# Performance work log

Measured on AMD Instinct MI355X. Metric: run time of the kernel, lower is better.

The kernel has to match this reference:

```python
import jax, jax.numpy as jnp
import numpy as np

B, S, D = 4, 2048, 512
E, K = 8, 2
MH = 4 * D      # resmlp mlp hidden
EH = 2 * D      # expert hidden
EPS = 1e-5


def setup_inputs() -> dict:
    key = jax.random.key(0)
    ks = jax.random.split(key, 16)
    s = 0.02
    return {
        "x": jax.random.normal(ks[0], (B, S, D), dtype=jnp.float32),
        "ln1_g": jnp.ones((D,), jnp.float32), "ln1_b": jnp.zeros((D,), jnp.float32),
        "w1": jax.random.normal(ks[1], (D, MH), jnp.float32) * s,
        "b1": jnp.zeros((MH,), jnp.float32),
        "w2": jax.random.normal(ks[2], (MH, D), jnp.float32) * s,
        "b2": jnp.zeros((D,), jnp.float32),
        "ln2_g": jnp.ones((D,), jnp.float32), "ln2_b": jnp.zeros((D,), jnp.float32),
        "wr": jax.random.normal(ks[3], (E, D), jnp.float32) * s,
        "ew1": jax.random.normal(ks[4], (E, D, EH), jnp.float32) * s,
        "eb1": jnp.zeros((E, EH), jnp.float32),
        "ew2": jax.random.normal(ks[5], (E, EH, D), jnp.float32) * s,
        "eb2": jnp.zeros((E, D), jnp.float32),
        "lnf_g": jnp.ones((D,), jnp.float32), "lnf_b": jnp.zeros((D,), jnp.float32),
    }


def _ln(z, g, b):
    m = z.mean(-1, keepdims=True)
    v = ((z - m) ** 2).mean(-1, keepdims=True)
    return (z - m) * jax.lax.rsqrt(v + EPS) * g + b


def reference(x, ln1_g, ln1_b, w1, b1, w2, b2, ln2_g, ln2_b,
              wr, ew1, eb1, ew2, eb2, lnf_g, lnf_b):
    # ---- ResidualMLPBlock (eval mode: dropout is identity) ----
    h = _ln(x, ln1_g, ln1_b)
    h = jax.nn.gelu(h @ w1 + b1, approximate=False) @ w2 + b2
    x = x + h
    x = _ln(x, ln2_g, ln2_b) + x
    # ---- MoE (eval: no jitter noise, aux_loss = 0) ----
    xf = x.reshape(-1, D)              # [N, D], N = B*S
    n = xf.shape[0]
    probs = jax.nn.softmax(xf @ wr.T, axis=-1)          # [N, E]
    topv, topi = jax.lax.top_k(probs, K)                # [N, K]
    topv = topv / topv.sum(-1, keepdims=True)
    # dense per-token gate per expert: sum over k of renormalized prob where idx==j
    gates = jnp.zeros((n, E), xf.dtype).at[jnp.arange(n)[:, None], topi].add(topv)
    # per-expert MLP over all tokens (masked scatter-combine via gates)
    he = jax.nn.gelu(jnp.einsum("nd,edh->enh", xf, ew1) + eb1[:, None, :],
                     approximate=False)                 # [E, N, 2D]
    ye = jnp.einsum("enh,ehd->end", he, ew2) + eb2[:, None, :]  # [E, N, D]
    out = jnp.einsum("ne,end->nd", gates, ye).reshape(B, S, D)
    # ---- final LayerNorm ----
    out = _ln(out, lnf_g, lnf_b)
    aux_loss = jnp.zeros((), x.dtype)  # eval mode
    return out, aux_loss
```

## Files before the change

kernel.cpp:

```cpp
#include <hip/hip_runtime.h>

#define NTOK 8192
#define DIM  512
#define MHID 2048
#define EHID 1024
#define NEXP 8
#define RBLK 64

using half_t = _Float16;
typedef _Float16 f16x8 __attribute__((ext_vector_type(8)));
typedef float    f32x16 __attribute__((ext_vector_type(16)));

#define MFMA32(a, b, c) __builtin_amdgcn_mfma_f32_32x32x16_f16((a), (b), (c), 0, 0, 0)

typedef const __attribute__((address_space(1))) void* gas_ptr;
typedef __attribute__((address_space(3))) void*       las_ptr;
__device__ __forceinline__ void gl16(const void* g, void* l) {
    __builtin_amdgcn_global_load_lds((gas_ptr)g, (las_ptr)l, 16, 0, 0);
}

__device__ __forceinline__ float gelu_exact(float v) {
    return 0.5f * v * (1.0f + erff(v * 0.70710678118654752f));
}

__device__ __forceinline__ float block_sum4(float v, float* red, int tid) {
#pragma unroll
    for (int off = 32; off; off >>= 1) v += __shfl_down(v, off);
    if ((tid & 63) == 0) red[tid >> 6] = v;
    __syncthreads();
    float r = red[0] + red[1] + red[2] + red[3];
    __syncthreads();
    return r;
}

__global__ __launch_bounds__(256) void ln1_split_kernel(
    const float* __restrict__ x, const float* __restrict__ g, const float* __restrict__ b,
    half_t* __restrict__ xh, half_t* __restrict__ xl)
{
    const int row = blockIdx.x, tid = threadIdx.x;
    __shared__ float red[4];
    const size_t base = (size_t)row * DIM;
    float2 v = reinterpret_cast<const float2*>(x + base)[tid];
    float mean = block_sum4(v.x + v.y, red, tid) * (1.0f / DIM);
    float d0 = v.x - mean, d1 = v.y - mean;
    float var = block_sum4(d0 * d0 + d1 * d1, red, tid) * (1.0f / DIM);
    float rstd = rsqrtf(var + 1e-5f);
    int d = tid * 2;
    float y0 = d0 * rstd * g[d]     + b[d];
    float y1 = d1 * rstd * g[d + 1] + b[d + 1];
    half_t h0 = (half_t)y0, h1 = (half_t)y1;
    xh[base + d] = h0;  xh[base + d + 1] = h1;
    xl[base + d]     = (half_t)(y0 - (float)h0);
    xl[base + d + 1] = (half_t)(y1 - (float)h1);
}

__global__ __launch_bounds__(256) void resid_ln2_kernel(
    const float* __restrict__ x, float* __restrict__ p0, const float* __restrict__ p1,
    const float* __restrict__ b2,
    const float* __restrict__ g, const float* __restrict__ b,
    half_t* __restrict__ x3h)
{
    const int row = blockIdx.x, tid = threadIdx.x;
    __shared__ float red[4];
    const size_t base = (size_t)row * DIM;
    float2 xv = reinterpret_cast<const float2*>(x + base)[tid];
    float2 h0 = reinterpret_cast<float2*>(p0 + base)[tid];
    float2 h1 = reinterpret_cast<const float2*>(p1 + base)[tid];
    float2 bb = reinterpret_cast<const float2*>(b2)[tid];
    float z0 = xv.x + h0.x + h1.x + bb.x, z1 = xv.y + h0.y + h1.y + bb.y;
    float mean = block_sum4(z0 + z1, red, tid) * (1.0f / DIM);
    float d0 = z0 - mean, d1 = z1 - mean;
    float var = block_sum4(d0 * d0 + d1 * d1, red, tid) * (1.0f / DIM);
    float rstd = rsqrtf(var + 1e-5f);
    int d = tid * 2;
    float y0 = d0 * rstd * g[d]     + b[d]     + z0;
    float y1 = d1 * rstd * g[d + 1] + b[d + 1] + z1;
    float2 o; o.x = y0; o.y = y1;
    reinterpret_cast<float2*>(p0 + base)[tid] = o;
    x3h[base + d]     = (half_t)y0;
    x3h[base + d + 1] = (half_t)y1;
}

__global__ void transpose_split_kernel(const float* __restrict__ in,
                                       half_t* __restrict__ oh, half_t* __restrict__ ol,
                                       int R, int C)
{
    __shared__ float t[32][33];
    const size_t mo = (size_t)blockIdx.z * (size_t)R * (size_t)C;
    const int c0 = blockIdx.x * 32, r0 = blockIdx.y * 32;
    const int tx = threadIdx.x, ty = threadIdx.y;
    for (int i = ty; i < 32; i += 8) t[i][tx] = in[mo + (size_t)(r0 + i) * C + c0 + tx];
    __syncthreads();
    for (int i = ty; i < 32; i += 8) {
        float v = t[tx][i];
        size_t o = mo + (size_t)(c0 + i) * R + r0 + tx;
        half_t h = (half_t)v;
        oh[o] = h;
        if (ol) ol[o] = (half_t)(v - (float)h);
    }
}

template <int EPI, int NREP>
__global__ __launch_bounds__(512, 2) void gemm8_kernel(
    const half_t* __restrict__ A0, const half_t* __restrict__ A1,
    const half_t* __restrict__ B0, const half_t* __restrict__ B1,
    const float* __restrict__ bias,
    float* __restrict__ Cf0, float* __restrict__ Cf1,
    half_t* __restrict__ Ch, half_t* __restrict__ Cl,
    int Nc, int K, int Ktile)
{
    constexpr int BN    = NREP * 128;
    constexpr int LOADS = 4 + 2 * NREP;
    constexpr int TOT   = 16384 + NREP * 8192;
    __shared__ __align__(16) half_t lds[2 * TOT];

    const int m0 = blockIdx.x * 256, n0 = blockIdx.y * BN;
    const int kbeg = blockIdx.z * Ktile;
    float* Cf = blockIdx.z ? Cf1 : Cf0;
    const int tid = threadIdx.x;
    const int lane = tid & 63, wid = tid >> 6;
    const int wr = wid >> 2, wc = wid & 3;
    const int l31 = lane & 31, l5 = lane >> 5;

    const half_t* gsrc[LOADS];
    {
        const half_t* A0p = A0 + (size_t)m0 * K + kbeg;
        const half_t* A1p = A1 + (size_t)m0 * K + kbeg;
        const half_t* B0p = B0 + (size_t)n0 * K + kbeg;
        const half_t* B1p = B1 + (size_t)n0 * K + kbeg;
#pragma unroll
        for (int i = 0; i < LOADS; i++) {
            int c = tid + 512 * i;
            const half_t* base; int cm;
            if (c < 1024)                  { base = A0p; cm = c; }
            else if (c < 2048)             { base = A1p; cm = c - 1024; }
            else if (c < 2048 + NREP * 512){ base = B0p; cm = c - 2048; }
            else                           { base = B1p; cm = c - 2048 - NREP * 512; }
            int r = cm >> 2, ss = (cm & 3) ^ ((r >> 1) & 3);
            gsrc[i] = base + (size_t)r * K + ss * 8;
        }
    }

    int oa[4][2], ob[NREP][2];
#pragma unroll
    for (int m = 0; m < 4; m++)
#pragma unroll
        for (int kh = 0; kh < 2; kh++) {
            int ra = wr * 128 + m * 32 + l31;
            oa[m][kh] = ra * 32 + (((l5 + 2 * kh) ^ ((ra >> 1) & 3)) << 3);
        }
#pragma unroll
    for (int n = 0; n < NREP; n++)
#pragma unroll
        for (int kh = 0; kh < 2; kh++) {
            int rb = wc * (NREP * 32) + n * 32 + l31;
            ob[n][kh] = rb * 32 + (((l5 + 2 * kh) ^ ((rb >> 1) & 3)) << 3);
        }

    f32x16 acc[4][NREP];
#pragma unroll
    for (int m = 0; m < 4; m++)
#pragma unroll
        for (int n = 0; n < NREP; n++)
#pragma unroll
            for (int q = 0; q < 16; q++) acc[m][n][q] = 0.f;

    auto stage = [&](int bsel, int kof) {
#pragma unroll
        for (int i = 0; i < LOADS; i++)
            gl16(gsrc[i] + kof, &lds[bsel * TOT + (tid + 512 * i) * 8]);
    };
    auto phase = [&](int p, int kh) {
        const half_t* buf = &lds[p ? TOT : 0];
        f16x8 ah[4], al[4], bh[NREP], bl[NREP];
#pragma unroll
        for (int m = 0; m < 4; m++) {
            ah[m] = *(const f16x8*)(buf + oa[m][kh]);
            al[m] = *(const f16x8*)(buf + 8192 + oa[m][kh]);
        }
#pragma unroll
        for (int n = 0; n < NREP; n++) {
            bh[n] = *(const f16x8*)(buf + 16384 + ob[n][kh]);
            bl[n] = *(const f16x8*)(buf + 16384 + BN * 32 + ob[n][kh]);
        }
        __builtin_amdgcn_s_setprio(1);
#pragma unroll
        for (int m = 0; m < 4; m++)
#pragma unroll
            for (int n = 0; n < NREP; n++) {
                acc[m][n] = MFMA32(ah[m], bh[n], acc[m][n]);
                acc[m][n] = MFMA32(al[m], bh[n], acc[m][n]);
                acc[m][n] = MFMA32(ah[m], bl[n], acc[m][n]);
            }
        __builtin_amdgcn_s_setprio(0);
    };

    const int nsteps = Ktile / 32;
    stage(0, 0);
#pragma unroll 1
    for (int s = 0; s < nsteps - 1; ++s) {
        stage((s + 1) & 1, (s + 1) * 32);
        if constexpr (NREP == 2) asm volatile("s_waitcnt vmcnt(8)" ::: "memory");
        else                     asm volatile("s_waitcnt vmcnt(6)" ::: "memory");
        __builtin_amdgcn_s_barrier();
        phase(s & 1, 0);
        __builtin_amdgcn_s_barrier();
        phase(s & 1, 1);
        __builtin_amdgcn_s_barrier();
    }
    asm volatile("s_waitcnt vmcnt(0)" ::: "memory");
    __builtin_amdgcn_s_barrier();
    phase((nsteps - 1) & 1, 0);
    __builtin_amdgcn_s_barrier();
    phase((nsteps - 1) & 1, 1);

    const int er = 4 * l5;
#pragma unroll
    for (int m = 0; m < 4; m++)
#pragma unroll
        for (int n = 0; n < NREP; n++) {
            int cc = n0 + wc * (NREP * 32) + n * 32 + l31;
            float bv = (EPI == 1) ? bias[cc] : 0.f;
#pragma unroll
            for (int reg = 0; reg < 16; reg++) {
                int rr = m0 + wr * 128 + m * 32 + er + 8 * (reg >> 2) + (reg & 3);
                float v = acc[m][n][reg] + bv;
                size_t o = (size_t)rr * Nc + cc;
                if (EPI == 1) {
                    float ge = gelu_exact(v);
                    half_t h = (half_t)ge;
                    Ch[o] = h;
                    Cl[o] = (half_t)(ge - (float)h);
                } else {
                    Cf[o] = v;
                }
            }
        }
}

__global__ __launch_bounds__(256) void router_kernel(
    const float* __restrict__ x3, const float* __restrict__ wrm,
    int* __restrict__ cnt, int* __restrict__ aid, float* __restrict__ gate)
{
    __shared__ float wl[NEXP][DIM];
    __shared__ int   texp[RBLK * 2];
    __shared__ float tgate[RBLK * 2];
    __shared__ int   lslot[RBLK * 2];
    __shared__ int   lcnt[NEXP], lbase[NEXP];
    const int tid = threadIdx.x;
    for (int i = tid; i < NEXP * DIM / 4; i += 256)
        reinterpret_cast<float4*>(&wl[0][0])[i] = reinterpret_cast<const float4*>(wrm)[i];
    if (tid < NEXP) lcnt[tid] = 0;
    __syncthreads();
    const int w = tid >> 6, lane = tid & 63;
#pragma unroll 1
    for (int t = 0; t < RBLK / 4; ++t) {
        const int lt = w * (RBLK / 4) + t;
        const int token = blockIdx.x * RBLK + lt;
        const float* xr = x3 + (size_t)token * DIM;
        float a[NEXP];
#pragma unroll
        for (int e = 0; e < NEXP; e++) a[e] = 0.f;
#pragma unroll
        for (int d0 = 0; d0 < DIM; d0 += 64) {
            float xv = xr[d0 + lane];
#pragma unroll
            for (int e = 0; e < NEXP; e++) a[e] += xv * wl[e][d0 + lane];
        }
#pragma unroll
        for (int e = 0; e < NEXP; e++)
#pragma unroll
            for (int off = 32; off; off >>= 1) a[e] += __shfl_xor(a[e], off);
        if (lane == 0) {
            int i1 = 0; float v1 = a[0];
#pragma unroll
            for (int e = 1; e < NEXP; e++) if (a[e] > v1) { v1 = a[e]; i1 = e; }
            int i2 = -1; float v2 = -3.4e38f;
#pragma unroll
            for (int e = 0; e < NEXP; e++) if (e != i1 && a[e] > v2) { v2 = a[e]; i2 = e; }
            float e2 = expf(v2 - v1);
            float g1 = 1.0f / (1.0f + e2);
            texp[lt * 2]      = i1; tgate[lt * 2]      = g1;
            texp[lt * 2 + 1]  = i2; tgate[lt * 2 + 1]  = 1.0f - g1;
        }
    }
    __syncthreads();
    if (tid < RBLK * 2) lslot[tid] = atomicAdd(&lcnt[texp[tid]], 1);
    __syncthreads();
    if (tid < NEXP) lbase[tid] = atomicAdd(&cnt[tid * 32], lcnt[tid]);
    __syncthreads();
    if (tid < RBLK * 2) {
        const int e = texp[tid];
        const int asg = blockIdx.x * (RBLK * 2) + tid;
        aid[e * NTOK + lbase[e] + lslot[tid]] = asg;
        gate[asg] = tgate[tid];
    }
}

__global__ __launch_bounds__(256) void egemm1_kernel(
    const half_t* __restrict__ X,
    const half_t* __restrict__ W,
    const float* __restrict__ eb1,
    const int* __restrict__ cnt, const int* __restrict__ aid,
    half_t* __restrict__ He)
{
    const int bid = blockIdx.x;
    const int e = bid >> 9, rem = bid & 511;
    const int mt = rem >> 3, nt = rem & 7;
    const int ne = cnt[e * 32];
    if (mt * 128 >= ne) return;
    __shared__ __align__(16) half_t As[2][128 * 32];
    __shared__ __align__(16) half_t Bs[2][128 * 32];
    __shared__ int rowmap[128];
    const int tid = threadIdx.x;
    if (tid < 128) {
        int slot = mt * 128 + tid;
        rowmap[tid] = (slot < ne) ? aid[e * NTOK + slot] : -1;
    }
    __syncthreads();
    const int lane = tid & 63, wid = tid >> 6;
    const int wr = wid >> 1, wc = wid & 1;
    const int c0 = tid, c1 = tid + 256;
    const int r0 = c0 >> 2, s0 = (c0 & 3) ^ ((r0 >> 1) & 3);
    const int r1 = c1 >> 2, s1 = (c1 & 3) ^ ((r1 >> 1) & 3);
    const int a0r = rowmap[r0], a1r = rowmap[r1];
    const half_t* pa0 = X + (size_t)(a0r >= 0 ? (a0r >> 1) : 0) * DIM + s0 * 8;
    const half_t* pa1 = X + (size_t)(a1r >= 0 ? (a1r >> 1) : 0) * DIM + s1 * 8;
    const half_t* pb0 = W + (size_t)e * EHID * DIM + (size_t)(nt * 128 + r0) * DIM + s0 * 8;
    const half_t* pb1 = W + (size_t)e * EHID * DIM + (size_t)(nt * 128 + r1) * DIM + s1 * 8;

    const int l31 = lane & 31, l5 = lane >> 5;
    int oa[2][2], ob[2][2];
#pragma unroll
    for (int i = 0; i < 2; i++)
#pragma unroll
        for (int kh = 0; kh < 2; kh++) {
            int ra = wr * 64 + i * 32 + l31;
            oa[i][kh] = ra * 32 + (((l5 + kh * 2) ^ ((ra >> 1) & 3)) << 3);
            int rb = wc * 64 + i * 32 + l31;
            ob[i][kh] = rb * 32 + (((l5 + kh * 2) ^ ((rb >> 1) & 3)) << 3);
        }
    f32x16 acc[2][2];
#pragma unroll
    for (int i = 0; i < 2; i++)
#pragma unroll
        for (int j = 0; j < 2; j++)
#pragma unroll
            for (int q = 0; q < 16; q++) acc[i][j][q] = 0.f;

    auto stage = [&](int bsel, int k0) {
        gl16(pa0 + k0, &As[bsel][c0 * 8]);
        gl16(pa1 + k0, &As[bsel][c1 * 8]);
        gl16(pb0 + k0, &Bs[bsel][c0 * 8]);
        gl16(pb1 + k0, &Bs[bsel][c1 * 8]);
    };
    auto compute = [&](int bsel) {
#pragma unroll
        for (int kh = 0; kh < 2; kh++) {
            f16x8 a0 = *(const f16x8*)(&As[bsel][0] + oa[0][kh]);
            f16x8 a1 = *(const f16x8*)(&As[bsel][0] + oa[1][kh]);
            f16x8 b0 = *(const f16x8*)(&Bs[bsel][0] + ob[0][kh]);
            f16x8 b1 = *(const f16x8*)(&Bs[bsel][0] + ob[1][kh]);
            acc[0][0] = MFMA32(a0, b0, acc[0][0]);
            acc[0][1] = MFMA32(a0, b1, acc[0][1]);
            acc[1][0] = MFMA32(a1, b0, acc[1][0]);
            acc[1][1] = MFMA32(a1, b1, acc[1][1]);
        }
    };

    stage(0, 0);
#pragma unroll 1
    for (int k0 = 0; k0 < DIM; k0 += 64) {
        __syncthreads();
        if (k0 + 32 < DIM) stage(1, k0 + 32);
        compute(0);
        __syncthreads();
        if (k0 + 64 < DIM) stage(0, k0 + 64);
        compute(1);
    }
    const int er = 4 * l5;
#pragma unroll
    for (int i = 0; i < 2; i++)
#pragma unroll
        for (int reg = 0; reg < 16; reg++) {
            int rloc = wr * 64 + i * 32 + er + 8 * (reg >> 2) + (reg & 3);
            int a = rowmap[rloc];
            if (a >= 0) {
#pragma unroll
                for (int j = 0; j < 2; j++) {
                    int cc = nt * 128 + wc * 64 + j * 32 + l31;
                    float v = acc[i][j][reg] + eb1[e * EHID + cc];
                    He[(size_t)a * EHID + cc] = (half_t)gelu_exact(v);
                }
            }
        }
}

__global__ __launch_bounds__(256) void egemm2_kernel(
    const half_t* __restrict__ Hin,
    const half_t* __restrict__ W,
    const float* __restrict__ eb2,
    const int* __restrict__ cnt, const int* __restrict__ aid,
    const float* __restrict__ gate,
    float* __restrict__ Ye)
{
    const int bid = blockIdx.x;
    const int e = bid >> 8, rem = bid & 255;
    const int mt = rem >> 2, nt = rem & 3;
    const int ne = cnt[e * 32];
    if (mt * 128 >= ne) return;
    __shared__ __align__(16) half_t As[2][128 * 32];
    __shared__ __align__(16) half_t Bs[2][128 * 32];
    __shared__ int rowmap[128];
    const int tid = threadIdx.x;
    if (tid < 128) {
        int slot = mt * 128 + tid;
        rowmap[tid] = (slot < ne) ? aid[e * NTOK + slot] : -1;
    }
    __syncthreads();
    const int lane = tid & 63, wid = tid >> 6;
    const int wr = wid >> 1, wc = wid & 1;
    const int c0 = tid, c1 = tid + 256;
    const int r0 = c0 >> 2, s0 = (c0 & 3) ^ ((r0 >> 1) & 3);
    const int r1 = c1 >> 2, s1 = (c1 & 3) ^ ((r1 >> 1) & 3);
    const int a0r = rowmap[r0], a1r = rowmap[r1];
    const half_t* pa0 = Hin + (size_t)(a0r >= 0 ? a0r : 0) * EHID + s0 * 8;
    const half_t* pa1 = Hin + (size_t)(a1r >= 0 ? a1r : 0) * EHID + s1 * 8;
    const half_t* pb0 = W + (size_t)e * DIM * EHID + (size_t)(nt * 128 + r0) * EHID + s0 * 8;
    const half_t* pb1 = W + (size_t)e * DIM * EHID + (size_t)(nt * 128 + r1) * EHID + s1 * 8;

    const int l31 = lane & 31, l5 = lane >> 5;
    int oa[2][2], ob[2][2];
#pragma unroll
    for (int i = 0; i < 2; i++)
#pragma unroll
        for (int kh = 0; kh < 2; kh++) {
            int ra = wr * 64 + i * 32 + l31;
            oa[i][kh] = ra * 32 + (((l5 + kh * 2) ^ ((ra >> 1) & 3)) << 3);
            int rb = wc * 64 + i * 32 + l31;
            ob[i][kh] = rb * 32 + (((l5 + kh * 2) ^ ((rb >> 1) & 3)) << 3);
        }
    f32x16 acc[2][2];
#pragma unroll
    for (int i = 0; i < 2; i++)
#pragma unroll
        for (int j = 0; j < 2; j++)
#pragma unroll
            for (int q = 0; q < 16; q++) acc[i][j][q] = 0.f;

    auto stage = [&](int bsel, int k0) {
        gl16(pa0 + k0, &As[bsel][c0 * 8]);
        gl16(pa1 + k0, &As[bsel][c1 * 8]);
        gl16(pb0 + k0, &Bs[bsel][c0 * 8]);
        gl16(pb1 + k0, &Bs[bsel][c1 * 8]);
    };
    auto compute = [&](int bsel) {
#pragma unroll
        for (int kh = 0; kh < 2; kh++) {
            f16x8 a0 = *(const f16x8*)(&As[bsel][0] + oa[0][kh]);
            f16x8 a1 = *(const f16x8*)(&As[bsel][0] + oa[1][kh]);
            f16x8 b0 = *(const f16x8*)(&Bs[bsel][0] + ob[0][kh]);
            f16x8 b1 = *(const f16x8*)(&Bs[bsel][0] + ob[1][kh]);
            acc[0][0] = MFMA32(a0, b0, acc[0][0]);
            acc[0][1] = MFMA32(a0, b1, acc[0][1]);
            acc[1][0] = MFMA32(a1, b0, acc[1][0]);
            acc[1][1] = MFMA32(a1, b1, acc[1][1]);
        }
    };

    stage(0, 0);
#pragma unroll 1
    for (int k0 = 0; k0 < EHID; k0 += 64) {
        __syncthreads();
        if (k0 + 32 < EHID) stage(1, k0 + 32);
        compute(0);
        __syncthreads();
        if (k0 + 64 < EHID) stage(0, k0 + 64);
        compute(1);
    }
    const int er = 4 * l5;
#pragma unroll
    for (int i = 0; i < 2; i++)
#pragma unroll
        for (int reg = 0; reg < 16; reg++) {
            int rloc = wr * 64 + i * 32 + er + 8 * (reg >> 2) + (reg & 3);
            int a = rowmap[rloc];
            if (a >= 0) {
                float gv = gate[a];
#pragma unroll
                for (int j = 0; j < 2; j++) {
                    int cc = nt * 128 + wc * 64 + j * 32 + l31;
                    float v = (acc[i][j][reg] + eb2[e * DIM + cc]) * gv;
                    Ye[(size_t)a * DIM + cc] = v;
                }
            }
        }
}

__global__ __launch_bounds__(256) void combine_lnf_kernel(
    const float* __restrict__ Ye, const float* __restrict__ g, const float* __restrict__ b,
    float* __restrict__ out)
{
    const int t = blockIdx.x, tid = threadIdx.x;
    __shared__ float red[4];
    float2 y0 = reinterpret_cast<const float2*>(Ye + (size_t)(2 * t) * DIM)[tid];
    float2 y1 = reinterpret_cast<const float2*>(Ye + (size_t)(2 * t + 1) * DIM)[tid];
    float z0 = y0.x + y1.x, z1 = y0.y + y1.y;
    float mean = block_sum4(z0 + z1, red, tid) * (1.0f / DIM);
    float d0 = z0 - mean, d1 = z1 - mean;
    float var = block_sum4(d0 * d0 + d1 * d1, red, tid) * (1.0f / DIM);
    float rstd = rsqrtf(var + 1e-5f);
    int d = tid * 2;
    out[(size_t)t * DIM + d]     = d0 * rstd * g[d]     + b[d];
    out[(size_t)t * DIM + d + 1] = d1 * rstd * g[d + 1] + b[d + 1];
    if (t == 0 && tid == 0) out[(size_t)NTOK * DIM] = 0.f;
}

__global__ void zero_cnt_kernel(int* cnt) {
    cnt[threadIdx.x] = 0;
}

extern "C" void kernel_launch(void* const* d_in, const int* in_sizes, int n_in,
                              void* d_out, int out_size, void* d_ws, size_t ws_size,
                              hipStream_t stream)
{
    (void)in_sizes; (void)n_in; (void)out_size; (void)ws_size;
    const float* x    = (const float*)d_in[0];
    const float* ln1g = (const float*)d_in[1];
    const float* ln1b = (const float*)d_in[2];
    const float* w1   = (const float*)d_in[3];
    const float* b1   = (const float*)d_in[4];
    const float* w2   = (const float*)d_in[5];
    const float* b2   = (const float*)d_in[6];
    const float* ln2g = (const float*)d_in[7];
    const float* ln2b = (const float*)d_in[8];
    const float* wrm  = (const float*)d_in[9];
    const float* ew1  = (const float*)d_in[10];
    const float* eb1  = (const float*)d_in[11];
    const float* ew2  = (const float*)d_in[12];
    const float* eb2  = (const float*)d_in[13];
    const float* lnfg = (const float*)d_in[14];
    const float* lnfb = (const float*)d_in[15];
    float* out = (float*)d_out;

    char* w = (char*)d_ws;
    size_t off = 0;
    auto take = [&](size_t bytes) {
        char* p = w + off;
        off += bytes;
        off = (off + 255) & ~(size_t)255;
        return p;
    };
    half_t* xh_h  = (half_t*)take((size_t)NTOK * DIM * 2);
    half_t* xh_l  = (half_t*)take((size_t)NTOK * DIM * 2);
    half_t* w1t_h = (half_t*)take((size_t)DIM * MHID * 2);
    half_t* w1t_l = (half_t*)take((size_t)DIM * MHID * 2);
    half_t* w2t_h = (half_t*)take((size_t)MHID * DIM * 2);
    half_t* w2t_l = (half_t*)take((size_t)MHID * DIM * 2);
    char*   big   = take((size_t)NTOK * MHID * 2 * 2);
    half_t* a1h   = (half_t*)big;
    half_t* a1l   = (half_t*)(big + (size_t)NTOK * MHID * 2);
    half_t* heh   = (half_t*)big;
    float*  yef   = (float*)(big + (size_t)NTOK * MHID * 2);
    float*  x3f   = (float*)take((size_t)NTOK * DIM * 4);
    half_t* x3h   = (half_t*)take((size_t)NTOK * DIM * 2);
    half_t* ew1t  = (half_t*)take((size_t)NEXP * DIM * EHID * 2);
    half_t* ew2t  = (half_t*)take((size_t)NEXP * EHID * DIM * 2);
    int*    cnt   = (int*)take(1024);
    int*    aid   = (int*)take((size_t)NEXP * NTOK * 4);
    float*  gate  = (float*)take((size_t)NTOK * 2 * 4);

    float* p0 = x3f;
    float* p1 = (float*)xh_h;

    zero_cnt_kernel<<<1, 256, 0, stream>>>(cnt);
    ln1_split_kernel<<<NTOK, 256, 0, stream>>>(x, ln1g, ln1b, xh_h, xh_l);
    transpose_split_kernel<<<dim3(MHID / 32, DIM / 32, 1), dim3(32, 8), 0, stream>>>(w1, w1t_h, w1t_l, DIM, MHID);
    transpose_split_kernel<<<dim3(DIM / 32, MHID / 32, 1), dim3(32, 8), 0, stream>>>(w2, w2t_h, w2t_l, MHID, DIM);
    transpose_split_kernel<<<dim3(EHID / 32, DIM / 32, NEXP), dim3(32, 8), 0, stream>>>(ew1, ew1t, (half_t*)0, DIM, EHID);
    transpose_split_kernel<<<dim3(DIM / 32, EHID / 32, NEXP), dim3(32, 8), 0, stream>>>(ew2, ew2t, (half_t*)0, EHID, DIM);
    gemm8_kernel<1, 2><<<dim3(NTOK / 256, MHID / 256, 1), 512, 0, stream>>>(
        xh_h, xh_l, w1t_h, w1t_l, b1, (float*)0, (float*)0, a1h, a1l, MHID, DIM, DIM);
    gemm8_kernel<0, 1><<<dim3(NTOK / 256, DIM / 128, 2), 512, 0, stream>>>(
        a1h, a1l, w2t_h, w2t_l, (const float*)0, p0, p1, (half_t*)0, (half_t*)0, DIM, MHID, MHID / 2);
    resid_ln2_kernel<<<NTOK, 256, 0, stream>>>(x, p0, p1, b2, ln2g, ln2b, x3h);
    router_kernel<<<NTOK / RBLK, 256, 0, stream>>>(x3f, wrm, cnt, aid, gate);
    egemm1_kernel<<<NEXP * (NTOK / 128) * (EHID / 128), 256, 0, stream>>>(x3h, ew1t, eb1, cnt, aid, heh);
    egemm2_kernel<<<NEXP * (NTOK / 128) * (DIM / 128), 256, 0, stream>>>(heh, ew2t, eb2, cnt, aid, gate, yef);
    combine_lnf_kernel<<<NTOK, 256, 0, stream>>>(yef, lnfg, lnfb, out);
}
```

Measured before the change: 320.2 us.

## Load GEMM B operands directly from global into registers, bypassing LDS

```diff
diff --git a/kernel.cpp b/kernel.cpp
--- a/kernel.cpp
+++ b/kernel.cpp
@@ -100,7 +100,7 @@
     }
 }
 
-template <int EPI, int NREP>
+template <int EPI, int WR, int NREP>
 __global__ __launch_bounds__(512, 2) void gemm8_kernel(
     const half_t* __restrict__ A0, const half_t* __restrict__ A1,
     const half_t* __restrict__ B0, const half_t* __restrict__ B1,
@@ -109,121 +109,137 @@
     half_t* __restrict__ Ch, half_t* __restrict__ Cl,
     int Nc, int K, int Ktile)
 {
-    constexpr int BN    = NREP * 128;
-    constexpr int LOADS = 4 + 2 * NREP;
-    constexpr int TOT   = 16384 + NREP * 8192;
-    __shared__ __align__(16) half_t lds[2 * TOT];
+    constexpr int WC = 8 / WR;
+    constexpr int WM = 8 / WR;
+    constexpr int BN = WC * NREP * 32;
+    __shared__ __align__(16) half_t lds[2 * 16384];
 
     const int m0 = blockIdx.x * 256, n0 = blockIdx.y * BN;
     const int kbeg = blockIdx.z * Ktile;
     float* Cf = blockIdx.z ? Cf1 : Cf0;
     const int tid = threadIdx.x;
     const int lane = tid & 63, wid = tid >> 6;
-    const int wr = wid >> 2, wc = wid & 3;
+    const int wr = wid / WC, wc = wid % WC;
     const int l31 = lane & 31, l5 = lane >> 5;
 
-    const half_t* gsrc[LOADS];
+    const half_t* gsrc[4];
     {
         const half_t* A0p = A0 + (size_t)m0 * K + kbeg;
         const half_t* A1p = A1 + (size_t)m0 * K + kbeg;
-        const half_t* B0p = B0 + (size_t)n0 * K + kbeg;
-        const half_t* B1p = B1 + (size_t)n0 * K + kbeg;
-#pragma unroll
-        for (int i = 0; i < LOADS; i++) {
+#pragma unroll
+        for (int i = 0; i < 4; i++) {
             int c = tid + 512 * i;
-            const half_t* base; int cm;
-            if (c < 1024)                  { base = A0p; cm = c; }
-            else if (c < 2048)             { base = A1p; cm = c - 1024; }
-            else if (c < 2048 + NREP * 512){ base = B0p; cm = c - 2048; }
-            else                           { base = B1p; cm = c - 2048 - NREP * 512; }
+            const half_t* base = (c < 1024) ? A0p : A1p;
+            int cm = c & 1023;
             int r = cm >> 2, ss = (cm & 3) ^ ((r >> 1) & 3);
             gsrc[i] = base + (size_t)r * K + ss * 8;
         }
     }
 
-    int oa[4][2], ob[NREP][2];
-#pragma unroll
-    for (int m = 0; m < 4; m++)
+    int oa[WM][2];
+#pragma unroll
+    for (int m = 0; m < WM; m++)
 #pragma unroll
         for (int kh = 0; kh < 2; kh++) {
-            int ra = wr * 128 + m * 32 + l31;
+            int ra = wr * (WM * 32) + m * 32 + l31;
             oa[m][kh] = ra * 32 + (((l5 + 2 * kh) ^ ((ra >> 1) & 3)) << 3);
         }
-#pragma unroll
-    for (int n = 0; n < NREP; n++)
-#pragma unroll
-        for (int kh = 0; kh < 2; kh++) {
-            int rb = wc * (NREP * 32) + n * 32 + l31;
-            ob[n][kh] = rb * 32 + (((l5 + 2 * kh) ^ ((rb >> 1) & 3)) << 3);
-        }
-
-    f32x16 acc[4][NREP];
-#pragma unroll
-    for (int m = 0; m < 4; m++)
+
+    const half_t* pbh[NREP];
+    const half_t* pbl[NREP];
+#pragma unroll
+    for (int n = 0; n < NREP; n++) {
+        int rb = n0 + wc * (NREP * 32) + n * 32 + l31;
+        size_t o = (size_t)rb * K + kbeg + l5 * 8;
+        pbh[n] = B0 + o;
+        pbl[n] = B1 + o;
+    }
+
+    struct BF { f16x8 h[2][NREP]; f16x8 l[2][NREP]; };
+    BF fA, fB;
+    auto loadB = [&](BF& f, int kof) {
+#pragma unroll
+        for (int kh = 0; kh < 2; kh++)
+#pragma unroll
+            for (int n = 0; n < NREP; n++) {
+                f.h[kh][n] = *(const f16x8*)(pbh[n] + kof + kh * 16);
+                f.l[kh][n] = *(const f16x8*)(pbl[n] + kof + kh * 16);
+            }
+    };
+
+    f32x16 acc[WM][NREP];
+#pragma unroll
+    for (int m = 0; m < WM; m++)
 #pragma unroll
         for (int n = 0; n < NREP; n++)
 #pragma unroll
             for (int q = 0; q < 16; q++) acc[m][n][q] = 0.f;
 
-    auto stage = [&](int bsel, int kof) {
-#pragma unroll
-        for (int i = 0; i < LOADS; i++)
-            gl16(gsrc[i] + kof, &lds[bsel * TOT + (tid + 512 * i) * 8]);
-    };
-    auto phase = [&](int p, int kh) {
-        const half_t* buf = &lds[p ? TOT : 0];
-        f16x8 ah[4], al[4], bh[NREP], bl[NREP];
-#pragma unroll
-        for (int m = 0; m < 4; m++) {
-            ah[m] = *(const f16x8*)(buf + oa[m][kh]);
-            al[m] = *(const f16x8*)(buf + 8192 + oa[m][kh]);
-        }
-#pragma unroll
-        for (int n = 0; n < NREP; n++) {
-            bh[n] = *(const f16x8*)(buf + 16384 + ob[n][kh]);
-            bl[n] = *(const f16x8*)(buf + 16384 + BN * 32 + ob[n][kh]);
-        }
+    auto stageA = [&](int bsel, int kof) {
+#pragma unroll
+        for (int i = 0; i < 4; i++)
+            gl16(gsrc[i] + kof, &lds[bsel * 16384 + (tid + 512 * i) * 8]);
+    };
+    auto phase = [&](const half_t* buf, int kh, const BF& f) {
         __builtin_amdgcn_s_setprio(1);
 #pragma unroll
-        for (int m = 0; m < 4; m++)
+        for (int m = 0; m < WM; m++) {
+            f16x8 ah = *(const f16x8*)(buf + oa[m][kh]);
+            f16x8 al = *(const f16x8*)(buf + 8192 + oa[m][kh]);
 #pragma unroll
             for (int n = 0; n < NREP; n++) {
-                acc[m][n] = MFMA32(ah[m], bh[n], acc[m][n]);
-                acc[m][n] = MFMA32(al[m], bh[n], acc[m][n]);
-                acc[m][n] = MFMA32(ah[m], bl[n], acc[m][n]);
+                acc[m][n] = MFMA32(ah, f.h[kh][n], acc[m][n]);
+                acc[m][n] = MFMA32(al, f.h[kh][n], acc[m][n]);
+                acc[m][n] = MFMA32(ah, f.l[kh][n], acc[m][n]);
             }
+        }
         __builtin_amdgcn_s_setprio(0);
     };
 
+    const half_t* buf0 = &lds[0];
+    const half_t* buf1 = &lds[16384];
     const int nsteps = Ktile / 32;
-    stage(0, 0);
+
+    stageA(0, 0); loadB(fA, 0);
 #pragma unroll 1
-    for (int s = 0; s < nsteps - 1; ++s) {
-        stage((s + 1) & 1, (s + 1) * 32);
-        if constexpr (NREP == 2) asm volatile("s_waitcnt vmcnt(8)" ::: "memory");
-        else                     asm volatile("s_waitcnt vmcnt(6)" ::: "memory");
+    for (int s = 0; s + 2 < nsteps; s += 2) {
+        stageA(1, (s + 1) * 32); loadB(fB, (s + 1) * 32);
+        asm volatile("s_waitcnt vmcnt(12)" ::: "memory");
         __builtin_amdgcn_s_barrier();
-        phase(s & 1, 0);
+        phase(buf0, 0, fA);
         __builtin_amdgcn_s_barrier();
-        phase(s & 1, 1);
+        phase(buf0, 1, fA);
         __builtin_amdgcn_s_barrier();
-    }
+        stageA(0, (s + 2) * 32); loadB(fA, (s + 2) * 32);
+        asm volatile("s_waitcnt vmcnt(12)" ::: "memory");
+        __builtin_amdgcn_s_barrier();
+        phase(buf1, 0, fB);
+        __builtin_amdgcn_s_barrier();
+        phase(buf1, 1, fB);
+        __builtin_amdgcn_s_barrier();
+    }
+    stageA(1, (nsteps - 1) * 32); loadB(fB, (nsteps - 1) * 32);
+    asm volatile("s_waitcnt vmcnt(12)" ::: "memory");
+    __builtin_amdgcn_s_barrier();
+    phase(buf0, 0, fA);
+    __builtin_amdgcn_s_barrier();
+    phase(buf0, 1, fA);
     asm volatile("s_waitcnt vmcnt(0)" ::: "memory");
     __builtin_amdgcn_s_barrier();
-    phase((nsteps - 1) & 1, 0);
+    phase(buf1, 0, fB);
     __builtin_amdgcn_s_barrier();
-    phase((nsteps - 1) & 1, 1);
+    phase(buf1, 1, fB);
 
     const int er = 4 * l5;
 #pragma unroll
-    for (int m = 0; m < 4; m++)
+    for (int m = 0; m < WM; m++)
 #pragma unroll
         for (int n = 0; n < NREP; n++) {
             int cc = n0 + wc * (NREP * 32) + n * 32 + l31;
             float bv = (EPI == 1) ? bias[cc] : 0.f;
 #pragma unroll
             for (int reg = 0; reg < 16; reg++) {
-                int rr = m0 + wr * 128 + m * 32 + er + 8 * (reg >> 2) + (reg & 3);
+                int rr = m0 + wr * (WM * 32) + m * 32 + er + 8 * (reg >> 2) + (reg & 3);
                 float v = acc[m][n][reg] + bv;
                 size_t o = (size_t)rr * Nc + cc;
                 if (EPI == 1) {
@@ -310,7 +326,6 @@
     const int ne = cnt[e * 32];
     if (mt * 128 >= ne) return;
     __shared__ __align__(16) half_t As[2][128 * 32];
-    __shared__ __align__(16) half_t Bs[2][128 * 32];
     __shared__ int rowmap[128];
     const int tid = threadIdx.x;
     if (tid < 128) {
@@ -320,25 +335,24 @@
     __syncthreads();
     const int lane = tid & 63, wid = tid >> 6;
     const int wr = wid >> 1, wc = wid & 1;
+    const int l31 = lane & 31, l5 = lane >> 5;
     const int c0 = tid, c1 = tid + 256;
     const int r0 = c0 >> 2, s0 = (c0 & 3) ^ ((r0 >> 1) & 3);
     const int r1 = c1 >> 2, s1 = (c1 & 3) ^ ((r1 >> 1) & 3);
     const int a0r = rowmap[r0], a1r = rowmap[r1];
     const half_t* pa0 = X + (size_t)(a0r >= 0 ? (a0r >> 1) : 0) * DIM + s0 * 8;
     const half_t* pa1 = X + (size_t)(a1r >= 0 ? (a1r >> 1) : 0) * DIM + s1 * 8;
-    const half_t* pb0 = W + (size_t)e * EHID * DIM + (size_t)(nt * 128 + r0) * DIM + s0 * 8;
-    const half_t* pb1 = W + (size_t)e * EHID * DIM + (size_t)(nt * 128 + r1) * DIM + s1 * 8;
-
-    const int l31 = lane & 31, l5 = lane >> 5;
-    int oa[2][2], ob[2][2];
+    const half_t* Wb = W + (size_t)e * EHID * DIM;
+    const half_t* pb0 = Wb + (size_t)(nt * 128 + wc * 64 + l31) * DIM + l5 * 8;
+    const half_t* pb1 = Wb + (size_t)(nt * 128 + wc * 64 + 32 + l31) * DIM + l5 * 8;
+
+    int oa[2][2];
 #pragma unroll
     for (int i = 0; i < 2; i++)
 #pragma unroll
         for (int kh = 0; kh < 2; kh++) {
             int ra = wr * 64 + i * 32 + l31;
             oa[i][kh] = ra * 32 + (((l5 + kh * 2) ^ ((ra >> 1) & 3)) << 3);
-            int rb = wc * 64 + i * 32 + l31;
-            ob[i][kh] = rb * 32 + (((l5 + kh * 2) ^ ((rb >> 1) & 3)) << 3);
         }
     f32x16 acc[2][2];
 #pragma unroll
@@ -351,16 +365,14 @@
     auto stage = [&](int bsel, int k0) {
         gl16(pa0 + k0, &As[bsel][c0 * 8]);
         gl16(pa1 + k0, &As[bsel][c1 * 8]);
-        gl16(pb0 + k0, &Bs[bsel][c0 * 8]);
-        gl16(pb1 + k0, &Bs[bsel][c1 * 8]);
-    };
-    auto compute = [&](int bsel) {
+    };
+    auto compute = [&](int bsel, int kg) {
 #pragma unroll
         for (int kh = 0; kh < 2; kh++) {
+            f16x8 b0 = *(const f16x8*)(pb0 + kg + kh * 16);
+            f16x8 b1 = *(const f16x8*)(pb1 + kg + kh * 16);
             f16x8 a0 = *(const f16x8*)(&As[bsel][0] + oa[0][kh]);
             f16x8 a1 = *(const f16x8*)(&As[bsel][0] + oa[1][kh]);
-            f16x8 b0 = *(const f16x8*)(&Bs[bsel][0] + ob[0][kh]);
-            f16x8 b1 = *(const f16x8*)(&Bs[bsel][0] + ob[1][kh]);
             acc[0][0] = MFMA32(a0, b0, acc[0][0]);
             acc[0][1] = MFMA32(a0, b1, acc[0][1]);
             acc[1][0] = MFMA32(a1, b0, acc[1][0]);
@@ -373,10 +385,10 @@
     for (int k0 = 0; k0 < DIM; k0 += 64) {
         __syncthreads();
         if (k0 + 32 < DIM) stage(1, k0 + 32);
-        compute(0);
+        compute(0, k0);
         __syncthreads();
         if (k0 + 64 < DIM) stage(0, k0 + 64);
-        compute(1);
+        compute(1, k0 + 32);
     }
     const int er = 4 * l5;
 #pragma unroll
@@ -410,7 +422,6 @@
     const int ne = cnt[e * 32];
     if (mt * 128 >= ne) return;
     __shared__ __align__(16) half_t As[2][128 * 32];
-    __shared__ __align__(16) half_t Bs[2][128 * 32];
     __shared__ int rowmap[128];
     const int tid = threadIdx.x;
     if (tid < 128) {
@@ -420,25 +431,24 @@
     __syncthreads();
     const int lane = tid & 63, wid = tid >> 6;
     const int wr = wid >> 1, wc = wid & 1;
+    const int l31 = lane & 31, l5 = lane >> 5;
     const int c0 = tid, c1 = tid + 256;
     const int r0 = c0 >> 2, s0 = (c0 & 3) ^ ((r0 >> 1) & 3);
     const int r1 = c1 >> 2, s1 = (c1 & 3) ^ ((r1 >> 1) & 3);
     const int a0r = rowmap[r0], a1r = rowmap[r1];
     const half_t* pa0 = Hin + (size_t)(a0r >= 0 ? a0r : 0) * EHID + s0 * 8;
     const half_t* pa1 = Hin + (size_t)(a1r >= 0 ? a1r : 0) * EHID + s1 * 8;
-    const half_t* pb0 = W + (size_t)e * DIM * EHID + (size_t)(nt * 128 + r0) * EHID + s0 * 8;
-    const half_t* pb1 = W + (size_t)e * DIM * EHID + (size_t)(nt * 128 + r1) * EHID + s1 * 8;
-
-    const int l31 = lane & 31, l5 = lane >> 5;
-    int oa[2][2], ob[2][2];
+    const half_t* Wb = W + (size_t)e * DIM * EHID;
+    const half_t* pb0 = Wb + (size_t)(nt * 128 + wc * 64 + l31) * EHID + l5 * 8;
+    const half_t* pb1 = Wb + (size_t)(nt * 128 + wc * 64 + 32 + l31) * EHID + l5 * 8;
+
+    int oa[2][2];
 #pragma unroll
     for (int i = 0; i < 2; i++)
 #pragma unroll
         for (int kh = 0; kh < 2; kh++) {
             int ra = wr * 64 + i * 32 + l31;
             oa[i][kh] = ra * 32 + (((l5 + kh * 2) ^ ((ra >> 1) & 3)) << 3);
-            int rb = wc * 64 + i * 32 + l31;
-            ob[i][kh] = rb * 32 + (((l5 + kh * 2) ^ ((rb >> 1) & 3)) << 3);
         }
     f32x16 acc[2][2];
 #pragma unroll
@@ -451,16 +461,14 @@
     auto stage = [&](int bsel, int k0) {
         gl16(pa0 + k0, &As[bsel][c0 * 8]);
         gl16(pa1 + k0, &As[bsel][c1 * 8]);
-        gl16(pb0 + k0, &Bs[bsel][c0 * 8]);
-        gl16(pb1 + k0, &Bs[bsel][c1 * 8]);
-    };
-    auto compute = [&](int bsel) {
+    };
+    auto compute = [&](int bsel, int kg) {
 #pragma unroll
         for (int kh = 0; kh < 2; kh++) {
+            f16x8 b0 = *(const f16x8*)(pb0 + kg + kh * 16);
+            f16x8 b1 = *(const f16x8*)(pb1 + kg + kh * 16);
             f16x8 a0 = *(const f16x8*)(&As[bsel][0] + oa[0][kh]);
             f16x8 a1 = *(const f16x8*)(&As[bsel][0] + oa[1][kh]);
-            f16x8 b0 = *(const f16x8*)(&Bs[bsel][0] + ob[0][kh]);
-            f16x8 b1 = *(const f16x8*)(&Bs[bsel][0] + ob[1][kh]);
             acc[0][0] = MFMA32(a0, b0, acc[0][0]);
             acc[0][1] = MFMA32(a0, b1, acc[0][1]);
             acc[1][0] = MFMA32(a1, b0, acc[1][0]);
@@ -473,10 +481,10 @@
     for (int k0 = 0; k0 < EHID; k0 += 64) {
         __syncthreads();
         if (k0 + 32 < EHID) stage(1, k0 + 32);
-        compute(0);
+        compute(0, k0);
         __syncthreads();
         if (k0 + 64 < EHID) stage(0, k0 + 64);
-        compute(1);
+        compute(1, k0 + 32);
     }
     const int er = 4 * l5;
 #pragma unroll
@@ -579,9 +587,9 @@
     transpose_split_kernel<<<dim3(DIM / 32, MHID / 32, 1), dim3(32, 8), 0, stream>>>(w2, w2t_h, w2t_l, MHID, DIM);
     transpose_split_kernel<<<dim3(EHID / 32, DIM / 32, NEXP), dim3(32, 8), 0, stream>>>(ew1, ew1t, (half_t*)0, DIM, EHID);
     transpose_split_kernel<<<dim3(DIM / 32, EHID / 32, NEXP), dim3(32, 8), 0, stream>>>(ew2, ew2t, (half_t*)0, EHID, DIM);
-    gemm8_kernel<1, 2><<<dim3(NTOK / 256, MHID / 256, 1), 512, 0, stream>>>(
+    gemm8_kernel<1, 2, 2><<<dim3(NTOK / 256, MHID / 256, 1), 512, 0, stream>>>(
         xh_h, xh_l, w1t_h, w1t_l, b1, (float*)0, (float*)0, a1h, a1l, MHID, DIM, DIM);
-    gemm8_kernel<0, 1><<<dim3(NTOK / 256, DIM / 128, 2), 512, 0, stream>>>(
+    gemm8_kernel<0, 4, 2><<<dim3(NTOK / 256, DIM / 128, 2), 512, 0, stream>>>(
         a1h, a1l, w2t_h, w2t_l, (const float*)0, p0, p1, (half_t*)0, (half_t*)0, DIM, MHID, MHID / 2);
     resid_ln2_kernel<<<NTOK, 256, 0, stream>>>(x, p0, p1, b2, ln2g, ln2b, x3h);
     router_kernel<<<NTOK / RBLK, 256, 0, stream>>>(x3f, wrm, cnt, aid, gate);
```

Measured after the change: 407.4 us. 27.2% more time.
